# Kernel tuning notes

Hardware: AMD Instinct MI355X
Metric: run time of the kernel (lower is better)

Reference implementation:

```python
import jax, jax.numpy as jnp
import numpy as np

EMBED = 1024
HEADS = 16
HEAD_DIM = EMBED // HEADS


def setup_inputs() -> dict:
    key = jax.random.key(0)
    ks = jax.random.split(key, 12)
    B, S, D = 4, 2048, EMBED
    scale = 1.0 / np.sqrt(D)
    inp = {
        "query": jax.random.normal(ks[0], (B, S, D), dtype=jnp.float32),
        "key": jax.random.normal(ks[1], (B, S, D), dtype=jnp.float32),
        "value": jax.random.normal(ks[2], (B, S, D), dtype=jnp.float32),
        "Wq": jax.random.normal(ks[3], (D, D), dtype=jnp.float32) * scale,
        "bq": jnp.zeros((D,), dtype=jnp.float32),
        "Wk": jax.random.normal(ks[4], (D, D), dtype=jnp.float32) * scale,
        "bk": jnp.zeros((D,), dtype=jnp.float32),
        "Wv": jax.random.normal(ks[5], (D, D), dtype=jnp.float32) * scale,
        "bv": jnp.zeros((D,), dtype=jnp.float32),
        "Wo": jax.random.normal(ks[6], (D, D), dtype=jnp.float32) * scale,
        "bo": jnp.zeros((D,), dtype=jnp.float32),
    }
    return inp


def reference(query, key, value, Wq, bq, Wk, bk, Wv, bv, Wo, bo):
    B, S, D = query.shape
    H, Dh = HEADS, HEAD_DIM

    def proj(x, W, b):
        # nn.Linear: x @ W.T + b, then split heads -> [B, H, S, Dh]
        y = jnp.einsum('bsd,ed->bse', x, W) + b
        return y.reshape(B, -1, H, Dh).transpose(0, 2, 1, 3)

    q = proj(query, Wq, bq)
    k = proj(key, Wk, bk)
    v = proj(value, Wv, bv)

    attn = jnp.einsum('bhqd,bhkd->bhqk', q, k) / jnp.sqrt(jnp.float32(Dh))
    attn = jax.nn.softmax(attn, axis=-1)
    # dropout: eval mode -> identity
    out = jnp.einsum('bhqk,bhkd->bhqd', attn, v)
    out = out.transpose(0, 2, 1, 3).reshape(B, -1, D)
    out = jnp.einsum('bsd,ed->bse', out, Wo) + bo
    return out
```

## Files before the change

kernel.cpp:

```cpp
#include <hip/hip_runtime.h>
#include <hip/hip_bf16.h>

typedef unsigned short u16;
typedef unsigned int u32;
typedef float f32x4 __attribute__((ext_vector_type(4)));
typedef float f32x16 __attribute__((ext_vector_type(16)));
typedef __bf16 bf16x8 __attribute__((ext_vector_type(8)));
typedef u32 u32x2 __attribute__((ext_vector_type(2)));

#define DEV static __device__ __forceinline__

DEV u16 f2b(float f) { __bf16 h = (__bf16)f; u16 r; __builtin_memcpy(&r, &h, 2); return r; }
DEV u32 pk2(float a, float b) { return (u32)f2b(a) | ((u32)f2b(b) << 16); }
DEV bf16x8 as_bf(uint4 v) { bf16x8 r; __builtin_memcpy(&r, &v, 16); return r; }

#define GLDS(g, l) __builtin_amdgcn_global_load_lds( \
    (__attribute__((address_space(1))) void*)(g),     \
    (__attribute__((address_space(3))) void*)(l), 16, 0, 0)

DEV void wb2() { asm volatile("s_waitcnt vmcnt(2)\n\ts_barrier" ::: "memory"); }
DEV void wb4() { asm volatile("s_waitcnt vmcnt(4)\n\ts_barrier" ::: "memory"); }
DEV void wb0() { asm volatile("s_waitcnt vmcnt(0)\n\ts_barrier" ::: "memory"); }

__global__ __launch_bounds__(256) void conva3_k(const float* __restrict__ s0,
                                                const float* __restrict__ s1,
                                                const float* __restrict__ s2,
                                                u16* __restrict__ dst, int n8)
{
  const int seg = blockIdx.y;
  const float* s = seg == 0 ? s0 : (seg == 1 ? s1 : s2);
  u16* d = dst + (size_t)seg * 8388608;
  const int stride = gridDim.x * 256;
  for (int i = blockIdx.x * 256 + threadIdx.x; i < n8; i += stride) {
    const float4* p = (const float4*)(s + (size_t)i * 8);
    const float4 a = p[0], b = p[1];
    *(uint4*)(d + (size_t)i * 8) =
        make_uint4(pk2(a.x, a.y), pk2(a.z, a.w), pk2(b.x, b.y), pk2(b.z, b.w));
  }
}

__global__ __launch_bounds__(256) void convw_k(const float* __restrict__ w0,
                                               const float* __restrict__ w1,
                                               const float* __restrict__ w2,
                                               const float* __restrict__ w3,
                                               u16* __restrict__ dst)
{
  const int seg = blockIdx.x >> 9, sb = blockIdx.x & 511;
  const float* s = seg == 0 ? w0 : seg == 1 ? w1 : seg == 2 ? w2 : w3;
  const int i = sb * 256 + threadIdx.x;
  const float4* p = (const float4*)(s + (size_t)i * 8);
  const float4 a = p[0], b = p[1];
  *(uint4*)(dst + (size_t)seg * 1048576 + (size_t)i * 8) =
      make_uint4(pk2(a.x, a.y), pk2(a.z, a.w), pk2(b.x, b.y), pk2(b.z, b.w));
}

__global__ __launch_bounds__(256) void gemm_qkv(const u16* __restrict__ Ac,
                                                const u16* __restrict__ Wc,
                                                const float* __restrict__ b0,
                                                const float* __restrict__ b1,
                                                const float* __restrict__ b2,
                                                u16* __restrict__ C0,
                                                u16* __restrict__ C1,
                                                u16* __restrict__ C2,
                                                float qscale)
{
  __shared__ u16 lds[2][8192];
  const int tid = threadIdx.x;
  const int lane = tid & 63, w = tid >> 6;
  const int f = blockIdx.x;
  const int xcd = f & 7, i = f >> 3;
  const int mg = i & 7, yz = i >> 3;
  const int m0 = (xcd * 8 + mg) * 128;
  const int z = yz >> 3, e0 = (yz & 7) * 128;
  const int wrb = (w >> 1) * 4, wcb = (w & 1) * 4;

  const u16* A = Ac + (size_t)z * 8388608;
  const u16* Wp = Wc + (size_t)z * 1048576;
  const float* bias = z == 0 ? b0 : (z == 1 ? b1 : b2);
  u16* Cp = z == 0 ? C0 : (z == 1 ? C1 : C2);
  const float scale = (z == 0) ? qscale : 1.0f;
  const int cmode = (z == 2) ? 3 : 2;

  f32x4 acc[4][4];
#pragma unroll
  for (int ii = 0; ii < 4; ii++)
#pragma unroll
    for (int j = 0; j < 4; j++)
#pragma unroll
      for (int r = 0; r < 4; r++) acc[ii][j][r] = 0.f;

  const u16* gA = A  + (size_t)(m0 + w * 32 + (lane & 15)) * 1024 + (lane >> 4) * 8;
  const u16* gB = Wp + (size_t)(e0 + w * 32 + (lane & 15)) * 1024 + (lane >> 4) * 8;

#define GSTAGE(K0, BUF)                                        \
  GLDS(gA + (K0),         &lds[BUF][w * 1024]);                \
  GLDS(gA + (K0) + 16384, &lds[BUF][w * 1024 + 512]);          \
  GLDS(gB + (K0),         &lds[BUF][4096 + w * 1024]);         \
  GLDS(gB + (K0) + 16384, &lds[BUF][4096 + w * 1024 + 512]);

  GSTAGE(0, 0)
  __syncthreads();

  const int fo = (lane >> 4) * 128 + (lane & 15) * 8;
  int buf = 0;
  for (int kb = 0; kb < 32; ++kb) {
    const int nbuf = buf ^ 1;
    if (kb < 31) { GSTAGE((kb + 1) * 32, nbuf) }
    {
      const u16* la = &lds[buf][0];
      const u16* lb = &lds[buf][4096];
      bf16x8 af[4], bfr[4];
#pragma unroll
      for (int ii = 0; ii < 4; ii++) {
        af[ii]  = as_bf(*(const uint4*)(la + (wrb + ii) * 512 + fo));
        bfr[ii] = as_bf(*(const uint4*)(lb + (wcb + ii) * 512 + fo));
      }
#pragma unroll
      for (int ii = 0; ii < 4; ii++)
#pragma unroll
        for (int j = 0; j < 4; j++)
          acc[ii][j] = __builtin_amdgcn_mfma_f32_16x16x32_bf16(af[ii], bfr[j],
                                                               acc[ii][j], 0, 0, 0);
    }
    __syncthreads();
    buf = nbuf;
  }
#undef GSTAGE

  const int col = lane & 15, rb4 = (lane >> 4) * 4;
  const int wr = wrb * 16, wc = wcb * 16;
#pragma unroll
  for (int j = 0; j < 4; j++) {
    const int e = e0 + wc + j * 16 + col;
    const float bv2 = bias[e];
#pragma unroll
    for (int ii = 0; ii < 4; ii++) {
#pragma unroll
      for (int r = 0; r < 4; r++) {
        const int m = m0 + wr + ii * 16 + rb4 + r;
        const float v = (acc[ii][j][r] + bv2) * scale;
        const int b = m >> 11, s = m & 2047, h = e >> 6, dh = e & 63;
        const size_t bh = (size_t)(b * 16 + h);
        if (cmode == 2) {
          const size_t idx = (((bh * 64 + (s >> 5)) * 4 + (dh >> 4)) * 64
                              + ((dh >> 3) & 1) * 32 + (s & 31)) * 8 + (dh & 7);
          Cp[idx] = f2b(v);
        } else {
          const size_t idx = ((bh * 64 + (s >> 5)) * 8 + ((s >> 4) & 1) * 4
                              + (dh >> 5) * 2 + ((s >> 3) & 1)) * 256
                             + (size_t)(dh & 31) * 8 + (s & 7);
          Cp[idx] = f2b(v);
        }
      }
    }
  }
}

__global__ __launch_bounds__(256) void gemm_o(const u16* __restrict__ A,
                                              const u16* __restrict__ W,
                                              const float* __restrict__ bias,
                                              float* __restrict__ Cp)
{
  __shared__ u16 lds[3][8192];
  const int tid = threadIdx.x;
  const int lane = tid & 63, w = tid >> 6;
  const int m0 = blockIdx.x * 128, e0 = blockIdx.y * 128;
  const int wrb = (w >> 1) * 4, wcb = (w & 1) * 4;

  f32x4 acc[4][4];
#pragma unroll
  for (int i = 0; i < 4; i++)
#pragma unroll
    for (int j = 0; j < 4; j++)
#pragma unroll
      for (int r = 0; r < 4; r++) acc[i][j][r] = 0.f;

  const u16* gA = A + (size_t)(m0 + w * 32 + (lane & 15)) * 1024 + (lane >> 4) * 8;
  const u16* gB = W + (size_t)(e0 + w * 32 + (lane & 15)) * 1024 + (lane >> 4) * 8;

#define GSTAGE(K0, BUF)                                        \
  GLDS(gA + (K0),         &lds[BUF][w * 1024]);                \
  GLDS(gA + (K0) + 16384, &lds[BUF][w * 1024 + 512]);          \
  GLDS(gB + (K0),         &lds[BUF][4096 + w * 1024]);         \
  GLDS(gB + (K0) + 16384, &lds[BUF][4096 + w * 1024 + 512]);

  GSTAGE(0, 0)
  GSTAGE(32, 1)

  const int fo = (lane >> 4) * 128 + (lane & 15) * 8;

#define GEMM_STEP(BUF)                                                         \
  {                                                                            \
    const u16* la = &lds[BUF][0];                                              \
    const u16* lb = &lds[BUF][4096];                                           \
    bf16x8 af[4], bfr[4];                                                      \
    _Pragma("unroll")                                                          \
    for (int i = 0; i < 4; i++) {                                              \
      af[i]  = as_bf(*(const uint4*)(la + (wrb + i) * 512 + fo));              \
      bfr[i] = as_bf(*(const uint4*)(lb + (wcb + i) * 512 + fo));              \
    }                                                                          \
    _Pragma("unroll")                                                          \
    for (int i = 0; i < 4; i++)                                                \
      _Pragma("unroll")                                                        \
      for (int j = 0; j < 4; j++)                                              \
        acc[i][j] = __builtin_amdgcn_mfma_f32_16x16x32_bf16(af[i], bfr[j],     \
                                                            acc[i][j], 0, 0, 0); \
  }

  for (int t = 0; t < 30; t += 3) {
    wb4(); GSTAGE((t + 2) * 32, 2) GEMM_STEP(0)
    wb4(); GSTAGE((t + 3) * 32, 0) GEMM_STEP(1)
    wb4(); GSTAGE((t + 4) * 32, 1) GEMM_STEP(2)
  }
  wb4(); GEMM_STEP(0)
  wb0(); GEMM_STEP(1)
#undef GEMM_STEP
#undef GSTAGE

  const int col = lane & 15, rb4 = (lane >> 4) * 4;
  const int wr = wrb * 16, wc = wcb * 16;
#pragma unroll
  for (int j = 0; j < 4; j++) {
    const int e = e0 + wc + j * 16 + col;
    const float bv = bias[e];
#pragma unroll
    for (int i = 0; i < 4; i++) {
#pragma unroll
      for (int r = 0; r < 4; r++) {
        const int m = m0 + wr + i * 16 + rb4 + r;
        Cp[(size_t)m * 1024 + e] = acc[i][j][r] + bv;
      }
    }
  }
}

__global__ __launch_bounds__(256, 4) void attn_k(const u16* __restrict__ Qb,
                                                 const u16* __restrict__ Kb,
                                                 const u16* __restrict__ Vb,
                                                 u16* __restrict__ O)
{
  __shared__ u16 pool[12288];
  const int tid = threadIdx.x, wv = tid >> 6, lane = tid & 63;
  const int lo = lane & 31, hi = lane >> 5;
  const int bid = blockIdx.x;
  const int xcd = bid & 7, ix = bid >> 3;
  const int bh = xcd * 8 + (ix & 7);
  const int qb = (ix >> 3) * 4 + wv;
  const int b = bh >> 4, h = bh & 15, q0 = qb * 32;

  const u16* qp = Qb + ((size_t)(bh * 64 + qb) * 4) * 512 + (size_t)lane * 8;
  bf16x8 qf[4];
#pragma unroll
  for (int c = 0; c < 4; c++) qf[c] = as_bf(*(const uint4*)(qp + c * 512));

  f32x16 a0, a1, zv;
#pragma unroll
  for (int r = 0; r < 16; r++) { a0[r] = 0.f; a1[r] = 0.f; zv[r] = 0.f; }
  float ls0 = 0.f, ls1 = 0.f;

  const u16* sgK = Kb + (size_t)bh * 131072 + wv * 512 + (size_t)lane * 8;
  const u16* sgV = Vb + (size_t)bh * 131072 + wv * 512 + (size_t)lane * 8;

#define ASTAGE(T, BUF)                                                  \
  GLDS(sgK + (size_t)(T) * 2048, pool + (BUF) * 4096 + wv * 512);       \
  GLDS(sgV + (size_t)(T) * 2048, pool + (BUF) * 4096 + 2048 + wv * 512);

  ASTAGE(0, 0)
  ASTAGE(1, 1)

#define ATTN_STEP(BUF)                                                        \
  {                                                                           \
    const u16* kl = pool + (BUF) * 4096;                                      \
    const u16* vl = kl + 2048;                                                \
    __builtin_amdgcn_s_setprio(1);                                            \
    f32x16 s = __builtin_amdgcn_mfma_f32_32x32x16_bf16(                       \
                 as_bf(*(const uint4*)(kl + lane * 8)), qf[0], zv, 0, 0, 0);  \
    _Pragma("unroll")                                                         \
    for (int c = 1; c < 4; c++)                                               \
      s = __builtin_amdgcn_mfma_f32_32x32x16_bf16(                            \
            as_bf(*(const uint4*)(kl + c * 512 + lane * 8)), qf[c], s, 0, 0, 0); \
    __builtin_amdgcn_s_setprio(0);                                            \
    _Pragma("unroll")                                                         \
    for (int r = 0; r < 16; r++) s[r] = __builtin_amdgcn_exp2f(s[r]);         \
    _Pragma("unroll")                                                         \
    for (int r = 0; r < 16; r += 2) { ls0 += s[r]; ls1 += s[r + 1]; }         \
    bf16x8 pf[2];                                                             \
    _Pragma("unroll")                                                         \
    for (int kc = 0; kc < 2; kc++) {                                          \
      const u32 A0 = pk2(s[8 * kc + 0], s[8 * kc + 1]);                       \
      const u32 A1 = pk2(s[8 * kc + 2], s[8 * kc + 3]);                       \
      const u32 B0 = pk2(s[8 * kc + 4], s[8 * kc + 5]);                       \
      const u32 B1 = pk2(s[8 * kc + 6], s[8 * kc + 7]);                       \
      u32x2 w02 = __builtin_amdgcn_permlane32_swap(A0, B0, false, false);     \
      u32x2 w13 = __builtin_amdgcn_permlane32_swap(A1, B1, false, false);     \
      pf[kc] = as_bf(make_uint4(w02[0], w13[0], w02[1], w13[1]));             \
    }                                                                         \
    __builtin_amdgcn_s_setprio(1);                                            \
    a0 = __builtin_amdgcn_mfma_f32_32x32x16_bf16(                             \
           as_bf(*(const uint4*)(vl + 0    + lane * 8)), pf[0], a0, 0, 0, 0); \
    a1 = __builtin_amdgcn_mfma_f32_32x32x16_bf16(                             \
           as_bf(*(const uint4*)(vl + 512  + lane * 8)), pf[0], a1, 0, 0, 0); \
    a0 = __builtin_amdgcn_mfma_f32_32x32x16_bf16(                             \
           as_bf(*(const uint4*)(vl + 1024 + lane * 8)), pf[1], a0, 0, 0, 0); \
    a1 = __builtin_amdgcn_mfma_f32_32x32x16_bf16(                             \
           as_bf(*(const uint4*)(vl + 1536 + lane * 8)), pf[1], a1, 0, 0, 0); \
    __builtin_amdgcn_s_setprio(0);                                            \
  }

  for (int t = 0; t < 60; t += 3) {
    wb2(); ASTAGE(t + 2, 2) ATTN_STEP(0)
    wb2(); ASTAGE(t + 3, 0) ATTN_STEP(1)
    wb2(); ASTAGE(t + 4, 1) ATTN_STEP(2)
  }
  wb2(); ASTAGE(62, 2) ATTN_STEP(0)
  wb2(); ASTAGE(63, 0) ATTN_STEP(1)
  wb2(); ATTN_STEP(2)
  wb0(); ATTN_STEP(0)
#undef ATTN_STEP
#undef ASTAGE

  __syncthreads();

  float l = ls0 + ls1;
  l += __shfl_xor(l, 32);
  const float inv = 1.f / l;
  u16* ob = pool + (wv * 32) * 72;

#pragma unroll
  for (int r = 0; r < 16; r++) {
    const int dh = (r & 3) + 8 * (r >> 2) + 4 * hi;
    ob[lo * 72 + dh]      = f2b(a0[r] * inv);
    ob[lo * 72 + dh + 32] = f2b(a1[r] * inv);
  }
  __builtin_amdgcn_s_barrier();
  const int qr = lane >> 1, hf = lane & 1;
  const u16* src = ob + qr * 72 + hf * 32;
  const uint4 r0 = *(const uint4*)(src + 0);
  const uint4 r1 = *(const uint4*)(src + 8);
  const uint4 r2 = *(const uint4*)(src + 16);
  const uint4 r3 = *(const uint4*)(src + 24);
  const size_t m = (size_t)b * 2048 + q0 + qr;
  uint4* dst = (uint4*)(O + m * 1024 + (size_t)h * 64 + hf * 32);
  dst[0] = r0; dst[1] = r1; dst[2] = r2; dst[3] = r3;
}

extern "C" void kernel_launch(void* const* d_in, const int* in_sizes, int n_in,
                              void* d_out, int out_size, void* d_ws, size_t ws_size,
                              hipStream_t stream)
{
  const float* query = (const float*)d_in[0];
  const float* key   = (const float*)d_in[1];
  const float* value = (const float*)d_in[2];
  const float* Wq = (const float*)d_in[3];
  const float* bq = (const float*)d_in[4];
  const float* Wk = (const float*)d_in[5];
  const float* bk = (const float*)d_in[6];
  const float* Wv = (const float*)d_in[7];
  const float* bv = (const float*)d_in[8];
  const float* Wo = (const float*)d_in[9];
  const float* bo = (const float*)d_in[10];

  const size_t MAT = (size_t)8192 * 1024;
  const size_t WMAT = (size_t)1024 * 1024;
  if (ws_size < (6 * MAT + 4 * WMAT) * sizeof(u16)) return;
  u16* Ac3 = (u16*)d_ws;
  u16* Wc  = Ac3 + 3 * MAT;
  u16* Qw  = Wc + 4 * WMAT;
  u16* Kw  = Qw + MAT;
  u16* Vw  = Kw + MAT;
  u16* Ow  = Ac3;

  const float qscale = 0.125f * 1.4426950408889634f;
  dim3 bl(256, 1, 1);

  hipLaunchKernelGGL(convw_k, dim3(2048), bl, 0, stream, Wq, Wk, Wv, Wo, Wc);
  hipLaunchKernelGGL(conva3_k, dim3(2048, 3), bl, 0, stream,
                     query, key, value, Ac3, (int)(MAT / 8));
  hipLaunchKernelGGL(gemm_qkv, dim3(1536), bl, 0, stream,
                     Ac3, Wc, bq, bk, bv, Qw, Kw, Vw, qscale);
  hipLaunchKernelGGL(attn_k, dim3(1024), bl, 0, stream, Qw, Kw, Vw, Ow);
  hipLaunchKernelGGL(gemm_o, dim3(64, 8), bl, 0, stream,
                     Ow, Wc + 3 * WMAT, bo, (float*)d_out);
}
```

Measured before the change: 255.6 us.

## Merge conversion kernels, triple-buffer QKV GEMM, double-tile attention staging

Folds the weight and activation fp32-to-bf16 conversions into a single launch. Gives the QKV GEMM a three-buffer LDS pipeline with vmcnt-based waits in place of a full sync every k-step, and changes its block-to-tile mapping from XCD-aware to linear. Switches attention from a three-buffer single-tile pipeline to a two-buffer pipeline that loads two K/V tiles per stage, with a full vmcnt(0) wait each stage. Together these cut launch and barrier overhead, but they raise LDS use and can reduce L2 locality and load/compute overlap in attention.

```diff
diff --git a/kernel.cpp b/kernel.cpp
--- a/kernel.cpp
+++ b/kernel.cpp
@@ -18,40 +18,39 @@
     (__attribute__((address_space(1))) void*)(g),     \
     (__attribute__((address_space(3))) void*)(l), 16, 0, 0)
 
-DEV void wb2() { asm volatile("s_waitcnt vmcnt(2)\n\ts_barrier" ::: "memory"); }
 DEV void wb4() { asm volatile("s_waitcnt vmcnt(4)\n\ts_barrier" ::: "memory"); }
 DEV void wb0() { asm volatile("s_waitcnt vmcnt(0)\n\ts_barrier" ::: "memory"); }
 
-__global__ __launch_bounds__(256) void conva3_k(const float* __restrict__ s0,
-                                                const float* __restrict__ s1,
-                                                const float* __restrict__ s2,
-                                                u16* __restrict__ dst, int n8)
-{
-  const int seg = blockIdx.y;
-  const float* s = seg == 0 ? s0 : (seg == 1 ? s1 : s2);
-  u16* d = dst + (size_t)seg * 8388608;
-  const int stride = gridDim.x * 256;
-  for (int i = blockIdx.x * 256 + threadIdx.x; i < n8; i += stride) {
-    const float4* p = (const float4*)(s + (size_t)i * 8);
+__global__ __launch_bounds__(256) void conv_all(const float* __restrict__ q,
+                                                const float* __restrict__ k,
+                                                const float* __restrict__ v,
+                                                const float* __restrict__ w0,
+                                                const float* __restrict__ w1,
+                                                const float* __restrict__ w2,
+                                                const float* __restrict__ w3,
+                                                u16* __restrict__ Ac3,
+                                                u16* __restrict__ Wc)
+{
+  const int y = blockIdx.y;
+  if (y < 3) {
+    const float* s = y == 0 ? q : (y == 1 ? k : v);
+    u16* d = Ac3 + (size_t)y * 8388608;
+    const int stride = gridDim.x * 256;
+    for (int i = blockIdx.x * 256 + threadIdx.x; i < 1048576; i += stride) {
+      const float4* p = (const float4*)(s + (size_t)i * 8);
+      const float4 a = p[0], b = p[1];
+      *(uint4*)(d + (size_t)i * 8) =
+          make_uint4(pk2(a.x, a.y), pk2(a.z, a.w), pk2(b.x, b.y), pk2(b.z, b.w));
+    }
+  } else {
+    const int i = blockIdx.x * 256 + threadIdx.x;
+    const int seg = i >> 17, off = i & 131071;
+    const float* s = seg == 0 ? w0 : seg == 1 ? w1 : seg == 2 ? w2 : w3;
+    const float4* p = (const float4*)(s + (size_t)off * 8);
     const float4 a = p[0], b = p[1];
-    *(uint4*)(d + (size_t)i * 8) =
+    *(uint4*)(Wc + (size_t)seg * 1048576 + (size_t)off * 8) =
         make_uint4(pk2(a.x, a.y), pk2(a.z, a.w), pk2(b.x, b.y), pk2(b.z, b.w));
   }
-}
-
-__global__ __launch_bounds__(256) void convw_k(const float* __restrict__ w0,
-                                               const float* __restrict__ w1,
-                                               const float* __restrict__ w2,
-                                               const float* __restrict__ w3,
-                                               u16* __restrict__ dst)
-{
-  const int seg = blockIdx.x >> 9, sb = blockIdx.x & 511;
-  const float* s = seg == 0 ? w0 : seg == 1 ? w1 : seg == 2 ? w2 : w3;
-  const int i = sb * 256 + threadIdx.x;
-  const float4* p = (const float4*)(s + (size_t)i * 8);
-  const float4 a = p[0], b = p[1];
-  *(uint4*)(dst + (size_t)seg * 1048576 + (size_t)i * 8) =
-      make_uint4(pk2(a.x, a.y), pk2(a.z, a.w), pk2(b.x, b.y), pk2(b.z, b.w));
 }
 
 __global__ __launch_bounds__(256) void gemm_qkv(const u16* __restrict__ Ac,
@@ -64,14 +63,12 @@
                                                 u16* __restrict__ C2,
                                                 float qscale)
 {
-  __shared__ u16 lds[2][8192];
+  __shared__ u16 lds[3][8192];
   const int tid = threadIdx.x;
   const int lane = tid & 63, w = tid >> 6;
   const int f = blockIdx.x;
-  const int xcd = f & 7, i = f >> 3;
-  const int mg = i & 7, yz = i >> 3;
-  const int m0 = (xcd * 8 + mg) * 128;
-  const int z = yz >> 3, e0 = (yz & 7) * 128;
+  const int z = f >> 9, r = f & 511;
+  const int m0 = (r & 63) * 128, e0 = (r >> 6) * 128;
   const int wrb = (w >> 1) * 4, wcb = (w & 1) * 4;
 
   const u16* A = Ac + (size_t)z * 8388608;
@@ -87,7 +84,7 @@
 #pragma unroll
     for (int j = 0; j < 4; j++)
 #pragma unroll
-      for (int r = 0; r < 4; r++) acc[ii][j][r] = 0.f;
+      for (int rr = 0; rr < 4; rr++) acc[ii][j][rr] = 0.f;
 
   const u16* gA = A  + (size_t)(m0 + w * 32 + (lane & 15)) * 1024 + (lane >> 4) * 8;
   const u16* gB = Wp + (size_t)(e0 + w * 32 + (lane & 15)) * 1024 + (lane >> 4) * 8;
@@ -99,32 +96,36 @@
   GLDS(gB + (K0) + 16384, &lds[BUF][4096 + w * 1024 + 512]);
 
   GSTAGE(0, 0)
-  __syncthreads();
+  GSTAGE(32, 1)
 
   const int fo = (lane >> 4) * 128 + (lane & 15) * 8;
-  int buf = 0;
-  for (int kb = 0; kb < 32; ++kb) {
-    const int nbuf = buf ^ 1;
-    if (kb < 31) { GSTAGE((kb + 1) * 32, nbuf) }
-    {
-      const u16* la = &lds[buf][0];
-      const u16* lb = &lds[buf][4096];
-      bf16x8 af[4], bfr[4];
-#pragma unroll
-      for (int ii = 0; ii < 4; ii++) {
-        af[ii]  = as_bf(*(const uint4*)(la + (wrb + ii) * 512 + fo));
-        bfr[ii] = as_bf(*(const uint4*)(lb + (wcb + ii) * 512 + fo));
-      }
-#pragma unroll
-      for (int ii = 0; ii < 4; ii++)
-#pragma unroll
-        for (int j = 0; j < 4; j++)
-          acc[ii][j] = __builtin_amdgcn_mfma_f32_16x16x32_bf16(af[ii], bfr[j],
-                                                               acc[ii][j], 0, 0, 0);
-    }
-    __syncthreads();
-    buf = nbuf;
-  }
+
+#define GEMM_STEP(BUF)                                                         \
+  {                                                                            \
+    const u16* la = &lds[BUF][0];                                              \
+    const u16* lb = &lds[BUF][4096];                                           \
+    bf16x8 af[4], bfr[4];                                                      \
+    _Pragma("unroll")                                                          \
+    for (int ii = 0; ii < 4; ii++) {                                           \
+      af[ii]  = as_bf(*(const uint4*)(la + (wrb + ii) * 512 + fo));            \
+      bfr[ii] = as_bf(*(const uint4*)(lb + (wcb + ii) * 512 + fo));            \
+    }                                                                          \
+    _Pragma("unroll")                                                          \
+    for (int ii = 0; ii < 4; ii++)                                             \
+      _Pragma("unroll")                                                        \
+      for (int j = 0; j < 4; j++)                                              \
+        acc[ii][j] = __builtin_amdgcn_mfma_f32_16x16x32_bf16(af[ii], bfr[j],   \
+                                                             acc[ii][j], 0, 0, 0); \
+  }
+
+  for (int t = 0; t < 30; t += 3) {
+    wb4(); GSTAGE((t + 2) * 32, 2) GEMM_STEP(0)
+    wb4(); GSTAGE((t + 3) * 32, 0) GEMM_STEP(1)
+    wb4(); GSTAGE((t + 4) * 32, 1) GEMM_STEP(2)
+  }
+  wb4(); GEMM_STEP(0)
+  wb0(); GEMM_STEP(1)
+#undef GEMM_STEP
 #undef GSTAGE
 
   const int col = lane & 15, rb4 = (lane >> 4) * 4;
@@ -136,9 +137,9 @@
 #pragma unroll
     for (int ii = 0; ii < 4; ii++) {
 #pragma unroll
-      for (int r = 0; r < 4; r++) {
-        const int m = m0 + wr + ii * 16 + rb4 + r;
-        const float v = (acc[ii][j][r] + bv2) * scale;
+      for (int rr = 0; rr < 4; rr++) {
+        const int m = m0 + wr + ii * 16 + rb4 + rr;
+        const float v = (acc[ii][j][rr] + bv2) * scale;
         const int b = m >> 11, s = m & 2047, h = e >> 6, dh = e & 63;
         const size_t bh = (size_t)(b * 16 + h);
         if (cmode == 2) {
@@ -239,7 +240,7 @@
                                                  const u16* __restrict__ Vb,
                                                  u16* __restrict__ O)
 {
-  __shared__ u16 pool[12288];
+  __shared__ u16 pool[16384];
   const int tid = threadIdx.x, wv = tid >> 6, lane = tid & 63;
   const int lo = lane & 31, hi = lane >> 5;
   const int bid = blockIdx.x;
@@ -261,17 +262,16 @@
   const u16* sgK = Kb + (size_t)bh * 131072 + wv * 512 + (size_t)lane * 8;
   const u16* sgV = Vb + (size_t)bh * 131072 + wv * 512 + (size_t)lane * 8;
 
-#define ASTAGE(T, BUF)                                                  \
-  GLDS(sgK + (size_t)(T) * 2048, pool + (BUF) * 4096 + wv * 512);       \
-  GLDS(sgV + (size_t)(T) * 2048, pool + (BUF) * 4096 + 2048 + wv * 512);
-
-  ASTAGE(0, 0)
-  ASTAGE(1, 1)
-
-#define ATTN_STEP(BUF)                                                        \
+#define ASTAGE2(T2, BUF)                                                       \
+  GLDS(sgK + (size_t)(2 * (T2))     * 2048, pool + (BUF) * 8192 +        wv * 512); \
+  GLDS(sgV + (size_t)(2 * (T2))     * 2048, pool + (BUF) * 8192 + 2048 + wv * 512); \
+  GLDS(sgK + (size_t)(2 * (T2) + 1) * 2048, pool + (BUF) * 8192 + 4096 + wv * 512); \
+  GLDS(sgV + (size_t)(2 * (T2) + 1) * 2048, pool + (BUF) * 8192 + 6144 + wv * 512);
+
+#define ATTN_TILE(KL, VL)                                                     \
   {                                                                           \
-    const u16* kl = pool + (BUF) * 4096;                                      \
-    const u16* vl = kl + 2048;                                                \
+    const u16* kl = (KL);                                                     \
+    const u16* vl = (VL);                                                     \
     __builtin_amdgcn_s_setprio(1);                                            \
     f32x16 s = __builtin_amdgcn_mfma_f32_32x32x16_bf16(                       \
                  as_bf(*(const uint4*)(kl + lane * 8)), qf[0], zv, 0, 0, 0);  \
@@ -307,17 +307,21 @@
     __builtin_amdgcn_s_setprio(0);                                            \
   }
 
-  for (int t = 0; t < 60; t += 3) {
-    wb2(); ASTAGE(t + 2, 2) ATTN_STEP(0)
-    wb2(); ASTAGE(t + 3, 0) ATTN_STEP(1)
-    wb2(); ASTAGE(t + 4, 1) ATTN_STEP(2)
-  }
-  wb2(); ASTAGE(62, 2) ATTN_STEP(0)
-  wb2(); ASTAGE(63, 0) ATTN_STEP(1)
-  wb2(); ATTN_STEP(2)
-  wb0(); ATTN_STEP(0)
-#undef ATTN_STEP
-#undef ASTAGE
+#define ATTN_STEP2(BUF)                                                       \
+  ATTN_TILE(pool + (BUF) * 8192,        pool + (BUF) * 8192 + 2048)           \
+  ATTN_TILE(pool + (BUF) * 8192 + 4096, pool + (BUF) * 8192 + 6144)
+
+  ASTAGE2(0, 0)
+  for (int t = 0; t < 31; ++t) {
+    wb0();
+    ASTAGE2(t + 1, (t & 1) ^ 1)
+    ATTN_STEP2(t & 1)
+  }
+  wb0();
+  ATTN_STEP2(1)
+#undef ATTN_STEP2
+#undef ATTN_TILE
+#undef ASTAGE2
 
   __syncthreads();
 
@@ -373,9 +377,8 @@
   const float qscale = 0.125f * 1.4426950408889634f;
   dim3 bl(256, 1, 1);
 
-  hipLaunchKernelGGL(convw_k, dim3(2048), bl, 0, stream, Wq, Wk, Wv, Wo, Wc);
-  hipLaunchKernelGGL(conva3_k, dim3(2048, 3), bl, 0, stream,
-                     query, key, value, Ac3, (int)(MAT / 8));
+  hipLaunchKernelGGL(conv_all, dim3(2048, 4), bl, 0, stream,
+                     query, key, value, Wq, Wk, Wv, Wo, Ac3, Wc);
   hipLaunchKernelGGL(gemm_qkv, dim3(1536), bl, 0, stream,
                      Ac3, Wc, bq, bk, bv, Qw, Kw, Vw, qscale);
   hipLaunchKernelGGL(attn_k, dim3(1024), bl, 0, stream, Qw, Kw, Vw, Ow);
```

After: 254.5 us, median of 5. Within noise of the previous version (-0.4%).
